# Optimization experiments

Hardware: AMD Instinct MI355X
Metric: run time of the kernel (lower is better)

## Reference

```python
import jax, jax.numpy as jnp
import numpy as np


def setup_inputs() -> dict:
    key = jax.random.key(0)
    k1, k2, k3 = jax.random.split(key, 3)
    B, N, L, H, E = 4, 4, 1024, 8, 64
    queries = jax.random.normal(k1, (B, N, L, H, E), dtype=jnp.float32)
    keys = jax.random.normal(k2, (B, N, L, H, E), dtype=jnp.float32)
    values = jax.random.normal(k3, (B, N, L, H, E), dtype=jnp.float32)
    return {"queries": queries, "keys": keys, "values": values}


def reference(queries, keys, values):
    B, N, L, H, E = queries.shape
    S = values.shape[2]
    scale = 1.0 / jnp.sqrt(jnp.asarray(E, queries.dtype))
    # scores: [B, N, H, L, S]
    scores = jnp.einsum('bnlhe,bnshe->bnhls', queries, keys)
    # causal mask: True above the diagonal (future positions), broadcast over b,n,h
    causal = jnp.triu(jnp.ones((L, S), dtype=bool), k=1)
    scores = jnp.where(causal, -jnp.inf, scores)
    A = jax.nn.softmax(scale * scores, axis=-1)  # dropout p=0.0 -> identity
    V = jnp.einsum('bnhls,bnshd->bnlhd', A, values)
    return V
```

## Files before the change

### kernel.cpp

```cpp
#include <hip/hip_runtime.h>
#include <hip/hip_bf16.h>


typedef __bf16 bf16x8 __attribute__((ext_vector_type(8)));
typedef __bf16 bf16x4 __attribute__((ext_vector_type(4)));
typedef float  f32x4  __attribute__((ext_vector_type(4)));

#define SEQ 1024
#define ROWSTRIDE 512
#define LDSPAD 72

__device__ inline bf16x8 pack8(float4 a, float4 b) {
    bf16x8 f;
    f[0]=(__bf16)a.x; f[1]=(__bf16)a.y; f[2]=(__bf16)a.z; f[3]=(__bf16)a.w;
    f[4]=(__bf16)b.x; f[5]=(__bf16)b.y; f[6]=(__bf16)b.z; f[7]=(__bf16)b.w;
    return f;
}

__device__ inline bf16x8 pack8s(float4 a, float4 b, float s) {
    bf16x8 f;
    f[0]=(__bf16)(a.x*s); f[1]=(__bf16)(a.y*s); f[2]=(__bf16)(a.z*s); f[3]=(__bf16)(a.w*s);
    f[4]=(__bf16)(b.x*s); f[5]=(__bf16)(b.y*s); f[6]=(__bf16)(b.z*s); f[7]=(__bf16)(b.w*s);
    return f;
}

__device__ inline void lds_barrier() {
    asm volatile("s_waitcnt lgkmcnt(0)\n\ts_barrier" ::: "memory");
}

__global__ __launch_bounds__(256) void attn_fwd(
    const float* __restrict__ Qg,
    const float* __restrict__ Kg,
    const float* __restrict__ Vg,
    float* __restrict__ Og)
{
    __shared__ __bf16 Kds[64][LDSPAD];
    __shared__ __bf16 Vds[64][LDSPAD];
    __shared__ __bf16 Pds[2][4][16][LDSPAD];

    const int blk  = blockIdx.x;
    const int pr   = blk >> 7;
    const int head = blk & 127;
    const int h    = head & 7;
    const int bn   = head >> 3;
    const int qts[2] = { pr, 15 - pr };

    const int tid  = threadIdx.x;
    const int wave = tid >> 6;
    const int lane = tid & 63;
    const int quad = lane >> 4;
    const int l15  = lane & 15;

    const size_t base = (size_t)bn * SEQ * ROWSTRIDE + (size_t)h * 64;

    const float kscale = 0.125f * 1.44269504088896f;

    bf16x8 qa[2][2];
    int qrow[2];
    #pragma unroll
    for (int st = 0; st < 2; ++st) {
        qrow[st] = qts[st] * 64 + wave * 16;
        const float* qp = Qg + base + (size_t)(qrow[st] + l15) * ROWSTRIDE + quad * 8;
        #pragma unroll
        for (int t = 0; t < 2; ++t)
            qa[st][t] = pack8s(*(const float4*)(qp + t * 32),
                               *(const float4*)(qp + t * 32 + 4), kscale);
    }

    f32x4 o[2][4];
    float lsum[2];
    #pragma unroll
    for (int st = 0; st < 2; ++st) {
        #pragma unroll
        for (int e = 0; e < 4; ++e) o[st][e] = (f32x4){0.f, 0.f, 0.f, 0.f};
        lsum[st] = 0.f;
    }

    const int sr = tid >> 2, sc = (tid & 3) << 4;
    const int ve = tid & 63, vs = (tid >> 6) << 4;

    const int ntiles = qts[1] + 1;

    const float* kbase = Kg + base;
    const float* vbase = Vg + base;

    float4 kpre[4];
    float  vpre[16];
    {
        const float* kp = kbase + (size_t)sr * ROWSTRIDE + sc;
        #pragma unroll
        for (int i = 0; i < 4; ++i) kpre[i] = *(const float4*)(kp + i * 4);
        const float* vp = vbase + (size_t)vs * ROWSTRIDE + ve;
        #pragma unroll
        for (int j = 0; j < 16; ++j) vpre[j] = vp[(size_t)j * ROWSTRIDE];
    }

    for (int tile = 0; tile < ntiles; ++tile) {
        lds_barrier();

        *(bf16x8*)&Kds[sr][sc]     = pack8(kpre[0], kpre[1]);
        *(bf16x8*)&Kds[sr][sc + 8] = pack8(kpre[2], kpre[3]);
        {
            bf16x8 f0, f1;
            #pragma unroll
            for (int jj = 0; jj < 8; ++jj) { f0[jj] = (__bf16)vpre[jj]; f1[jj] = (__bf16)vpre[8 + jj]; }
            *(bf16x8*)&Vds[ve][vs]     = f0;
            *(bf16x8*)&Vds[ve][vs + 8] = f1;
        }

        if (tile + 1 < ntiles) {
            const int s0n = (tile + 1) * 64;
            const float* kp = kbase + (size_t)(s0n + sr) * ROWSTRIDE + sc;
            #pragma unroll
            for (int i = 0; i < 4; ++i) kpre[i] = *(const float4*)(kp + i * 4);
            const float* vp = vbase + (size_t)(s0n + vs) * ROWSTRIDE + ve;
            #pragma unroll
            for (int j = 0; j < 16; ++j) vpre[j] = vp[(size_t)j * ROWSTRIDE];
        }

        lds_barrier();

        #pragma unroll
        for (int st = 0; st < 2; ++st) {
            if (tile > qts[st]) continue;
            f32x4 sacc[4];
            #pragma unroll
            for (int c = 0; c < 4; ++c) {
                sacc[c] = (f32x4){0.f, 0.f, 0.f, 0.f};
                #pragma unroll
                for (int t = 0; t < 2; ++t) {
                    bf16x8 kb = *(const bf16x8*)&Kds[c * 16 + l15][t * 32 + quad * 8];
                    sacc[c] = __builtin_amdgcn_mfma_f32_16x16x32_bf16(kb, qa[st][t], sacc[c], 0, 0, 0);
                }
            }
            const bool diag = (tile == qts[st]);
            const int qin = wave * 16 + l15;
            float ls = 0.f;
            #pragma unroll
            for (int c = 0; c < 4; ++c) {
                bf16x4 pk;
                #pragma unroll
                for (int r = 0; r < 4; ++r) {
                    float p = __builtin_amdgcn_exp2f(sacc[c][r]);
                    if (diag && (c * 16 + quad * 4 + r > qin)) p = 0.f;
                    ls += p;
                    pk[r] = (__bf16)p;
                }
                *(bf16x4*)&Pds[st][wave][l15][c * 16 + quad * 4] = pk;
            }
            lsum[st] += ls;
        }

        asm volatile("s_waitcnt lgkmcnt(0)" ::: "memory");

        const bool both = (tile <= qts[0]);
        #pragma unroll
        for (int e = 0; e < 4; ++e) {
            #pragma unroll
            for (int t = 0; t < 2; ++t) {
                bf16x8 vb = *(const bf16x8*)&Vds[e * 16 + l15][t * 32 + quad * 8];
                if (both) {
                    bf16x8 pb0 = *(const bf16x8*)&Pds[0][wave][l15][t * 32 + quad * 8];
                    o[0][e] = __builtin_amdgcn_mfma_f32_16x16x32_bf16(vb, pb0, o[0][e], 0, 0, 0);
                }
                bf16x8 pb1 = *(const bf16x8*)&Pds[1][wave][l15][t * 32 + quad * 8];
                o[1][e] = __builtin_amdgcn_mfma_f32_16x16x32_bf16(vb, pb1, o[1][e], 0, 0, 0);
            }
        }
    }

    #pragma unroll
    for (int st = 0; st < 2; ++st) {
        float s = lsum[st];
        s += __shfl_xor(s, 16);
        s += __shfl_xor(s, 32);
        const float inv_l = 1.f / s;
        float* op = Og + base + (size_t)(qrow[st] + l15) * ROWSTRIDE + quad * 4;
        #pragma unroll
        for (int e = 0; e < 4; ++e) {
            float4 v;
            v.x = o[st][e][0] * inv_l;
            v.y = o[st][e][1] * inv_l;
            v.z = o[st][e][2] * inv_l;
            v.w = o[st][e][3] * inv_l;
            *(float4*)(op + e * 16) = v;
        }
    }
}

extern "C" void kernel_launch(void* const* d_in, const int* in_sizes, int n_in,
                              void* d_out, int out_size, void* d_ws, size_t ws_size,
                              hipStream_t stream) {
    const float* Qg = (const float*)d_in[0];
    const float* Kg = (const float*)d_in[1];
    const float* Vg = (const float*)d_in[2];
    float* Og = (float*)d_out;
    attn_fwd<<<dim3(1024), dim3(256), 0, stream>>>(Qg, Kg, Vg, Og);
}
```

Baseline: 162.4 us.

## Use 32x32x16 MFMA with both query tiles packed per wave, P kept in registers

Switches from 16x16x32 to 32x32x16 bf16 MFMA. Each wave's 32 columns now cover 16 rows from each of the paired query tiles, so one MFMA processes both causal-pair tiles at once. The softmax probabilities are rearranged across half-waves with lane shuffles instead of a round trip through LDS, which removes the P shared buffer and its wait. The cost is that MFMAs are issued even for tiles past the short query tile (masked to zero), and the shuffle and packing logic is more complex.

```diff
diff --git a/kernel.cpp b/kernel.cpp
--- a/kernel.cpp
+++ b/kernel.cpp
@@ -3,8 +3,8 @@
 
 
 typedef __bf16 bf16x8 __attribute__((ext_vector_type(8)));
-typedef __bf16 bf16x4 __attribute__((ext_vector_type(4)));
-typedef float  f32x4  __attribute__((ext_vector_type(4)));
+typedef float  f32x16 __attribute__((ext_vector_type(16)));
+typedef unsigned int u32x4 __attribute__((ext_vector_type(4)));
 
 #define SEQ 1024
 #define ROWSTRIDE 512
@@ -16,12 +16,16 @@
     f[4]=(__bf16)b.x; f[5]=(__bf16)b.y; f[6]=(__bf16)b.z; f[7]=(__bf16)b.w;
     return f;
 }
-
 __device__ inline bf16x8 pack8s(float4 a, float4 b, float s) {
     bf16x8 f;
     f[0]=(__bf16)(a.x*s); f[1]=(__bf16)(a.y*s); f[2]=(__bf16)(a.z*s); f[3]=(__bf16)(a.w*s);
     f[4]=(__bf16)(b.x*s); f[5]=(__bf16)(b.y*s); f[6]=(__bf16)(b.z*s); f[7]=(__bf16)(b.w*s);
     return f;
+}
+__device__ inline unsigned int packbf2(float a, float b) {
+    unsigned short ua = __builtin_bit_cast(unsigned short, (__bf16)a);
+    unsigned short ub = __builtin_bit_cast(unsigned short, (__bf16)b);
+    return (unsigned int)ua | ((unsigned int)ub << 16);
 }
 
 __device__ inline void lds_barrier() {
@@ -36,51 +40,50 @@
 {
     __shared__ __bf16 Kds[64][LDSPAD];
     __shared__ __bf16 Vds[64][LDSPAD];
-    __shared__ __bf16 Pds[2][4][16][LDSPAD];
 
     const int blk  = blockIdx.x;
     const int pr   = blk >> 7;
     const int head = blk & 127;
-    const int h    = head & 7;
+    const int h_   = head & 7;
     const int bn   = head >> 3;
-    const int qts[2] = { pr, 15 - pr };
+    const int qt0  = pr, qt1 = 15 - pr;
 
     const int tid  = threadIdx.x;
     const int wave = tid >> 6;
     const int lane = tid & 63;
-    const int quad = lane >> 4;
+    const int hh   = lane >> 5;
+    const int l31  = lane & 31;
     const int l15  = lane & 15;
-
-    const size_t base = (size_t)bn * SEQ * ROWSTRIDE + (size_t)h * 64;
+    const int state = l31 >> 4;
+
+    const size_t base = (size_t)bn * SEQ * ROWSTRIDE + (size_t)h_ * 64;
+
+    const int qt_lane   = state ? qt1 : qt0;
+    const int q_in_tile = wave * 16 + l15;
+    const int qrow_lane = qt_lane * 64 + q_in_tile;
 
     const float kscale = 0.125f * 1.44269504088896f;
 
-    bf16x8 qa[2][2];
-    int qrow[2];
+    bf16x8 qf[4];
+    {
+        const float* qp = Qg + base + (size_t)qrow_lane * ROWSTRIDE + 8 * hh;
+        #pragma unroll
+        for (int ks = 0; ks < 4; ++ks)
+            qf[ks] = pack8s(*(const float4*)(qp + 16 * ks),
+                            *(const float4*)(qp + 16 * ks + 4), kscale);
+    }
+
+    f32x16 o[2];
     #pragma unroll
-    for (int st = 0; st < 2; ++st) {
-        qrow[st] = qts[st] * 64 + wave * 16;
-        const float* qp = Qg + base + (size_t)(qrow[st] + l15) * ROWSTRIDE + quad * 8;
-        #pragma unroll
-        for (int t = 0; t < 2; ++t)
-            qa[st][t] = pack8s(*(const float4*)(qp + t * 32),
-                               *(const float4*)(qp + t * 32 + 4), kscale);
-    }
-
-    f32x4 o[2][4];
-    float lsum[2];
-    #pragma unroll
-    for (int st = 0; st < 2; ++st) {
-        #pragma unroll
-        for (int e = 0; e < 4; ++e) o[st][e] = (f32x4){0.f, 0.f, 0.f, 0.f};
-        lsum[st] = 0.f;
-    }
+    for (int et = 0; et < 2; ++et)
+        #pragma unroll
+        for (int i = 0; i < 16; ++i) o[et][i] = 0.f;
+    float lsum = 0.f;
 
     const int sr = tid >> 2, sc = (tid & 3) << 4;
     const int ve = tid & 63, vs = (tid >> 6) << 4;
 
-    const int ntiles = qts[1] + 1;
-
+    const int ntiles = qt1 + 1;
     const float* kbase = Kg + base;
     const float* vbase = Vg + base;
 
@@ -120,70 +123,69 @@
 
         lds_barrier();
 
-        #pragma unroll
-        for (int st = 0; st < 2; ++st) {
-            if (tile > qts[st]) continue;
-            f32x4 sacc[4];
-            #pragma unroll
-            for (int c = 0; c < 4; ++c) {
-                sacc[c] = (f32x4){0.f, 0.f, 0.f, 0.f};
+        const int slimit = (tile < qt_lane) ? 64
+                         : ((tile == qt_lane) ? q_in_tile : -1);
+
+        #pragma unroll
+        for (int st2 = 0; st2 < 2; ++st2) {
+            f32x16 s16;
+            #pragma unroll
+            for (int i = 0; i < 16; ++i) s16[i] = 0.f;
+            #pragma unroll
+            for (int ks = 0; ks < 4; ++ks) {
+                bf16x8 kb = *(const bf16x8*)&Kds[st2 * 32 + l31][ks * 16 + 8 * hh];
+                s16 = __builtin_amdgcn_mfma_f32_32x32x16_bf16(kb, qf[ks], s16, 0, 0, 0);
+            }
+            unsigned int Dp[8];
+            float ps[16];
+            #pragma unroll
+            for (int reg = 0; reg < 16; ++reg) {
+                const int s_in = st2 * 32 + (reg & 3) + 8 * (reg >> 2) + 4 * hh;
+                float p = (s_in <= slimit) ? __builtin_amdgcn_exp2f(s16[reg]) : 0.f;
+                lsum += p;
+                ps[reg] = p;
+            }
+            #pragma unroll
+            for (int i = 0; i < 8; ++i) Dp[i] = packbf2(ps[2 * i], ps[2 * i + 1]);
+
+            #pragma unroll
+            for (int kh = 0; kh < 2; ++kh) {
+                const int ks = st2 * 2 + kh;
+                const int ka = 4 * kh;
+                unsigned int own0 = hh ? Dp[ka + 2] : Dp[ka + 0];
+                unsigned int own1 = hh ? Dp[ka + 3] : Dp[ka + 1];
+                unsigned int snd0 = hh ? Dp[ka + 0] : Dp[ka + 2];
+                unsigned int snd1 = hh ? Dp[ka + 1] : Dp[ka + 3];
+                unsigned int x0 = (unsigned int)__shfl_xor((int)snd0, 32);
+                unsigned int x1 = (unsigned int)__shfl_xor((int)snd1, 32);
+                u32x4 g;
+                g[0] = hh ? x0 : own0;
+                g[1] = hh ? x1 : own1;
+                g[2] = hh ? own0 : x0;
+                g[3] = hh ? own1 : x1;
+                bf16x8 pf = __builtin_bit_cast(bf16x8, g);
                 #pragma unroll
-                for (int t = 0; t < 2; ++t) {
-                    bf16x8 kb = *(const bf16x8*)&Kds[c * 16 + l15][t * 32 + quad * 8];
-                    sacc[c] = __builtin_amdgcn_mfma_f32_16x16x32_bf16(kb, qa[st][t], sacc[c], 0, 0, 0);
+                for (int et = 0; et < 2; ++et) {
+                    bf16x8 vb = *(const bf16x8*)&Vds[et * 32 + l31][ks * 16 + 8 * hh];
+                    o[et] = __builtin_amdgcn_mfma_f32_32x32x16_bf16(vb, pf, o[et], 0, 0, 0);
                 }
             }
-            const bool diag = (tile == qts[st]);
-            const int qin = wave * 16 + l15;
-            float ls = 0.f;
-            #pragma unroll
-            for (int c = 0; c < 4; ++c) {
-                bf16x4 pk;
-                #pragma unroll
-                for (int r = 0; r < 4; ++r) {
-                    float p = __builtin_amdgcn_exp2f(sacc[c][r]);
-                    if (diag && (c * 16 + quad * 4 + r > qin)) p = 0.f;
-                    ls += p;
-                    pk[r] = (__bf16)p;
-                }
-                *(bf16x4*)&Pds[st][wave][l15][c * 16 + quad * 4] = pk;
-            }
-            lsum[st] += ls;
-        }
-
-        asm volatile("s_waitcnt lgkmcnt(0)" ::: "memory");
-
-        const bool both = (tile <= qts[0]);
-        #pragma unroll
-        for (int e = 0; e < 4; ++e) {
-            #pragma unroll
-            for (int t = 0; t < 2; ++t) {
-                bf16x8 vb = *(const bf16x8*)&Vds[e * 16 + l15][t * 32 + quad * 8];
-                if (both) {
-                    bf16x8 pb0 = *(const bf16x8*)&Pds[0][wave][l15][t * 32 + quad * 8];
-                    o[0][e] = __builtin_amdgcn_mfma_f32_16x16x32_bf16(vb, pb0, o[0][e], 0, 0, 0);
-                }
-                bf16x8 pb1 = *(const bf16x8*)&Pds[1][wave][l15][t * 32 + quad * 8];
-                o[1][e] = __builtin_amdgcn_mfma_f32_16x16x32_bf16(vb, pb1, o[1][e], 0, 0, 0);
-            }
-        }
-    }
-
+        }
+    }
+
+    lsum += __shfl_xor(lsum, 32);
+    const float inv_l = 1.f / lsum;
+    float* op = Og + base + (size_t)qrow_lane * ROWSTRIDE + 4 * hh;
     #pragma unroll
-    for (int st = 0; st < 2; ++st) {
-        float s = lsum[st];
-        s += __shfl_xor(s, 16);
-        s += __shfl_xor(s, 32);
-        const float inv_l = 1.f / s;
-        float* op = Og + base + (size_t)(qrow[st] + l15) * ROWSTRIDE + quad * 4;
-        #pragma unroll
-        for (int e = 0; e < 4; ++e) {
+    for (int et = 0; et < 2; ++et) {
+        #pragma unroll
+        for (int g = 0; g < 4; ++g) {
             float4 v;
-            v.x = o[st][e][0] * inv_l;
-            v.y = o[st][e][1] * inv_l;
-            v.z = o[st][e][2] * inv_l;
-            v.w = o[st][e][3] * inv_l;
-            *(float4*)(op + e * 16) = v;
+            v.x = o[et][4 * g + 0] * inv_l;
+            v.y = o[et][4 * g + 1] * inv_l;
+            v.z = o[et][4 * g + 2] * inv_l;
+            v.w = o[et][4 * g + 3] * inv_l;
+            *(float4*)(op + et * 32 + g * 8) = v;
         }
     }
 }
```

Measured after the change: 170.5 us. +5.0%, slower.
